# Kernel tuning notes

Measured on AMD Instinct MI355X. Metric: run time of the kernel, lower is better.

The kernel has to match this reference:

```python
import jax, jax.numpy as jnp
import numpy as np

N = 256
IL_MMI = 0.02      # insertion loss MMI
IMB = 0.01         # imbalance MMI
IL_CR = 0.02       # insertion loss Crossing
CT = 0.01          # cross talk Crossing


def _mmi_matrix():
    # 2x2 MMI: sqrt(1-IL)*[[t, i r],[i r, t]] with t=sqrt((1+imb)/2), r=sqrt((1-imb)/2)
    a = np.sqrt(1.0 - IL_MMI)
    t = np.sqrt((1.0 + IMB) / 2.0)
    r = np.sqrt((1.0 - IMB) / 2.0)
    mmi2 = a * np.array([[t, 1j * r], [1j * r, t]], dtype=np.complex64)
    # block-diagonal over even pairs (0,1),(2,3),...
    return jnp.asarray(np.kron(np.eye(N // 2, dtype=np.complex64), mmi2))


def _crossing_matrix():
    # pairs start at odd index 1; rows 0 and N-1 pass through with amplitude sqrt(1-IL)*sqrt(1-CT)
    a = np.sqrt(1.0 - IL_CR)
    thru = a * np.sqrt(1.0 - CT)
    cr2 = a * np.array([[np.sqrt(CT), 1j * np.sqrt(1.0 - CT)],
                        [1j * np.sqrt(1.0 - CT), np.sqrt(CT)]], dtype=np.complex64)
    M = np.zeros((N, N), dtype=np.complex64)
    M[0, 0] = thru
    for i in range(1, N - 1, 2):
        M[i:i + 2, i:i + 2] = cr2
    if N % 2 == 0:
        M[-1, -1] = thru
    return jnp.asarray(M)


def setup_inputs() -> dict:
    key = jax.random.key(0)
    thetas = jax.random.uniform(key, (N // 2 + 2, N), dtype=jnp.float32) * (2.0 * np.pi)
    return {"thetas": thetas}


def reference(thetas):
    MMI = _mmi_matrix()
    CR = _crossing_matrix()
    phases = jnp.exp(1j * thetas)  # [N//2+2, N] complex64; diag phase-shift layers

    # arch = ht[0] @ I  (diagonal left-multiply == row scaling)
    arch0 = jnp.diag(phases[0])

    def body(arch, ph):
        # one mesh stage with trailing crossing (iterations i = 0 .. N//2-2)
        arch = MMI @ arch
        arch = ph[:, None] * arch      # ht[i+1] @ arch
        arch = MMI @ arch
        arch = CR @ arch
        return arch, None

    arch, _ = jax.lax.scan(body, arch0, phases[1:N // 2])

    # last loop iteration (i = N//2-1): no crossing
    arch = MMI @ arch
    arch = phases[N // 2][:, None] * arch
    arch = MMI @ arch
    # final phase layer ht[N//2+1]
    arch = phases[N // 2 + 1][:, None] * arch
    return arch
```

## Files before the change

### kernel.cpp

```cpp
#include <hip/hip_runtime.h>


__device__ __forceinline__ void sincos4(float4 th, float sn[4], float cs[4]) {
    __sincosf(th.x, &sn[0], &cs[0]);
    __sincosf(th.y, &sn[1], &cs[1]);
    __sincosf(th.z, &sn[2], &cs[2]);
    __sincosf(th.w, &sn[3], &cs[3]);
}

__global__ __launch_bounds__(64)
void neuropuls_mesh_kernel(const float* __restrict__ thetas,
                           float* __restrict__ out)
{
    constexpr int N = 256;
    const int lane = threadIdx.x;
    const int col  = blockIdx.x;

    const float AT = sqrtf(0.98f * 0.505f);
    const float AR = sqrtf(0.98f * 0.495f);
    const float BT = sqrtf(0.98f * 0.01f);
    const float BR = sqrtf(0.98f * 0.99f);

    float vr[4] = {0.f, 0.f, 0.f, 0.f};
    float vi[4] = {0.f, 0.f, 0.f, 0.f};

    {
        const float th0 = thetas[col];
        float s0, c0;
        __sincosf(th0, &s0, &c0);
        const int r0 = col - 4 * lane;
        if (0 <= r0 && r0 < 4) { vr[r0] = c0; vi[r0] = s0; }
    }

    const float* tp = thetas + N + 4 * lane;

    auto mmi_pair = [&](int x, int y) {
        float xr = vr[x], xi = vi[x], yr = vr[y], yi = vi[y];
        vr[x] = AT * xr - AR * yi;  vi[x] = AT * xi + AR * yr;
        vr[y] = AT * yr - AR * xi;  vi[y] = AT * yi + AR * xr;
    };
    auto phase4c = [&](const float sn[4], const float cs[4]) {
        #pragma unroll
        for (int j = 0; j < 4; ++j) {
            float r = vr[j], i = vi[j];
            vr[j] = cs[j] * r - sn[j] * i;
            vi[j] = cs[j] * i + sn[j] * r;
        }
    };
    auto crossing = [&]() {
        float pv3r = __shfl_up(vr[3], 1);
        float pv3i = __shfl_up(vi[3], 1);
        float nv0r = __shfl_down(vr[0], 1);
        float nv0i = __shfl_down(vi[0], 1);
        {
            float xr = vr[1], xi = vi[1], yr = vr[2], yi = vi[2];
            vr[1] = BT * xr - BR * yi;  vi[1] = BT * xi + BR * yr;
            vr[2] = BT * yr - BR * xi;  vi[2] = BT * yi + BR * xr;
        }
        {
            float yr = vr[0], yi = vi[0];
            float nr = BT * yr - BR * pv3i;
            float ni = BT * yi + BR * pv3r;
            vr[0] = (lane == 0) ? BR * yr : nr;
            vi[0] = (lane == 0) ? BR * yi : ni;
        }
        {
            float xr = vr[3], xi = vi[3];
            float nr = BT * xr - BR * nv0i;
            float ni = BT * xi + BR * nv0r;
            vr[3] = (lane == 63) ? BR * xr : nr;
            vi[3] = (lane == 63) ? BR * xi : ni;
        }
    };

    float snA[4], csA[4];
    float4 thN;
    {
        float4 t1 = *(const float4*)tp;  tp += N;
        thN = *(const float4*)tp;        tp += N;
        sincos4(t1, snA, csA);
    }

    #pragma unroll 2
    for (int s = 1; s <= 126; ++s) {
        float4 thNN = *(const float4*)tp;  tp += N;
        float snB[4], csB[4];
        sincos4(thN, snB, csB);
        mmi_pair(0, 1); mmi_pair(2, 3);
        phase4c(snA, csA);
        mmi_pair(0, 1); mmi_pair(2, 3);
        crossing();
        #pragma unroll
        for (int j = 0; j < 4; ++j) { snA[j] = snB[j]; csA[j] = csB[j]; }
        thN = thNN;
    }

    mmi_pair(0, 1); mmi_pair(2, 3);
    phase4c(snA, csA);
    mmi_pair(0, 1); mmi_pair(2, 3);
    crossing();

    {
        float sn[4], cs[4];
        sincos4(thN, sn, cs);
        float4 thF = *(const float4*)tp;
        mmi_pair(0, 1); mmi_pair(2, 3);
        phase4c(sn, cs);
        mmi_pair(0, 1); mmi_pair(2, 3);
        sincos4(thF, sn, cs);
        phase4c(sn, cs);
    }

    #pragma unroll
    for (int j = 0; j < 4; ++j) {
        const int idx = (4 * lane + j) * N + col;
        out[idx]         = vr[j];
        out[N * N + idx] = vi[j];
    }
}

extern "C" void kernel_launch(void* const* d_in, const int* in_sizes, int n_in,
                              void* d_out, int out_size, void* d_ws, size_t ws_size,
                              hipStream_t stream)
{
    const float* thetas = (const float*)d_in[0];
    float* out = (float*)d_out;
    (void)in_sizes; (void)n_in; (void)out_size; (void)d_ws; (void)ws_size;
    neuropuls_mesh_kernel<<<dim3(256), dim3(64), 0, stream>>>(thetas, out);
}
```

Before: 77.39 us.

## Split mesh chain into two half-chains and combine with complex matmul

Splits the serial 127-stage mesh propagation into two independent halves. One set of blocks propagates each input column through the first 64 stages, and another set propagates identity columns through the remaining stages. A second kernel multiplies the two 256x256 complex results to form the output. This halves the serial dependency chain and doubles the block count for better occupancy. In exchange it adds a full dense complex matrix product (N^3 work), a workspace round trip and a second launch.

```diff
diff --git a/kernel.cpp b/kernel.cpp
--- a/kernel.cpp
+++ b/kernel.cpp
@@ -1,20 +1,16 @@
 #include <hip/hip_runtime.h>
 
 
-__device__ __forceinline__ void sincos4(float4 th, float sn[4], float cs[4]) {
-    __sincosf(th.x, &sn[0], &cs[0]);
-    __sincosf(th.y, &sn[1], &cs[1]);
-    __sincosf(th.z, &sn[2], &cs[2]);
-    __sincosf(th.w, &sn[3], &cs[3]);
-}
+constexpr int N = 256;
 
 __global__ __launch_bounds__(64)
-void neuropuls_mesh_kernel(const float* __restrict__ thetas,
-                           float* __restrict__ out)
+void neuropuls_chain_kernel(const float* __restrict__ thetas,
+                            float2* __restrict__ Abuf,
+                            float2* __restrict__ Bbuf)
 {
-    constexpr int N = 256;
     const int lane = threadIdx.x;
-    const int col  = blockIdx.x;
+    const bool isB = blockIdx.x >= 256;
+    const int col  = blockIdx.x & 255;
 
     const float AT = sqrtf(0.98f * 0.505f);
     const float AR = sqrtf(0.98f * 0.495f);
@@ -25,14 +21,21 @@
     float vi[4] = {0.f, 0.f, 0.f, 0.f};
 
     {
-        const float th0 = thetas[col];
-        float s0, c0;
-        __sincosf(th0, &s0, &c0);
         const int r0 = col - 4 * lane;
-        if (0 <= r0 && r0 < 4) { vr[r0] = c0; vi[r0] = s0; }
+        if (0 <= r0 && r0 < 4) {
+            if (isB) { vr[r0] = 1.f; vi[r0] = 0.f; }
+            else {
+                float s0, c0;
+                __sincosf(thetas[col], &s0, &c0);
+                vr[r0] = c0; vi[r0] = s0;
+            }
+        }
     }
 
-    const float* tp = thetas + N + 4 * lane;
+    const int s0     = isB ? 65 : 1;
+    const int nCross = isB ? 63 : 64;
+
+    const float* tp = thetas + s0 * N + 4 * lane;
 
     auto mmi_pair = [&](int x, int y) {
         float xr = vr[x], xi = vi[x], yr = vr[y], yi = vi[y];
@@ -72,6 +75,12 @@
             vi[3] = (lane == 63) ? BR * xi : ni;
         }
     };
+    auto sincos4 = [](float4 th, float sn[4], float cs[4]) {
+        __sincosf(th.x, &sn[0], &cs[0]);
+        __sincosf(th.y, &sn[1], &cs[1]);
+        __sincosf(th.z, &sn[2], &cs[2]);
+        __sincosf(th.w, &sn[3], &cs[3]);
+    };
 
     float snA[4], csA[4];
     float4 thN;
@@ -82,7 +91,7 @@
     }
 
     #pragma unroll 2
-    for (int s = 1; s <= 126; ++s) {
+    for (int it = 0; it < nCross - 1; ++it) {
         float4 thNN = *(const float4*)tp;  tp += N;
         float snB[4], csB[4];
         sincos4(thN, snB, csB);
@@ -100,23 +109,45 @@
     mmi_pair(0, 1); mmi_pair(2, 3);
     crossing();
 
-    {
+    if (isB) {
         float sn[4], cs[4];
         sincos4(thN, sn, cs);
-        float4 thF = *(const float4*)tp;
         mmi_pair(0, 1); mmi_pair(2, 3);
         phase4c(sn, cs);
         mmi_pair(0, 1); mmi_pair(2, 3);
+        float4 thF = *(const float4*)(thetas + 129 * N + 4 * lane);
         sincos4(thF, sn, cs);
         phase4c(sn, cs);
     }
 
+    float2* dst = (isB ? Bbuf : Abuf) + col * N + 4 * lane;
     #pragma unroll
-    for (int j = 0; j < 4; ++j) {
-        const int idx = (4 * lane + j) * N + col;
-        out[idx]         = vr[j];
-        out[N * N + idx] = vi[j];
+    for (int j = 0; j < 4; ++j) dst[j] = make_float2(vr[j], vi[j]);
+}
+
+__global__ __launch_bounds__(256)
+void neuropuls_combine_kernel(const float2* __restrict__ Abuf,
+                              const float2* __restrict__ Bbuf,
+                              float* __restrict__ out)
+{
+    __shared__ float2 Acol[N];
+    const int c = blockIdx.x;
+    const int r = threadIdx.x;
+
+    Acol[r] = Abuf[c * N + r];
+    __syncthreads();
+
+    float accr = 0.f, acci = 0.f;
+    #pragma unroll 8
+    for (int k = 0; k < N; ++k) {
+        float2 b = Bbuf[k * N + r];
+        float2 a = Acol[k];
+        accr += b.x * a.x - b.y * a.y;
+        acci += b.x * a.y + b.y * a.x;
     }
+
+    out[r * N + c]         = accr;
+    out[N * N + r * N + c] = acci;
 }
 
 extern "C" void kernel_launch(void* const* d_in, const int* in_sizes, int n_in,
@@ -124,7 +155,11 @@
                               hipStream_t stream)
 {
     const float* thetas = (const float*)d_in[0];
+    float2* Abuf = (float2*)d_ws;
+    float2* Bbuf = Abuf + N * N;
     float* out = (float*)d_out;
-    (void)in_sizes; (void)n_in; (void)out_size; (void)d_ws; (void)ws_size;
-    neuropuls_mesh_kernel<<<dim3(256), dim3(64), 0, stream>>>(thetas, out);
+    (void)in_sizes; (void)n_in; (void)out_size; (void)ws_size;
+
+    neuropuls_chain_kernel<<<dim3(512), dim3(64), 0, stream>>>(thetas, Abuf, Bbuf);
+    neuropuls_combine_kernel<<<dim3(256), dim3(256), 0, stream>>>(Abuf, Bbuf, out);
 }
```

Result: slower. 85.43 us (+10.4%).
